# Kernel optimization log

Measured on AMD Instinct MI355X. Metric: run time of the kernel, lower is better.

## Reference

```python
import jax, jax.numpy as jnp
import numpy as np

N_USER = 25000
N_ITEM = 25000
N = N_USER + N_ITEM
E = 1_250_000
D = 64
L = 3
B = 4096


def setup_inputs() -> dict:
    key = jax.random.key(0)
    ks = jax.random.split(key, 11)
    emb = jax.random.normal(ks[0], (N, D), dtype=jnp.float32) * 0.1
    w1_w = jax.random.normal(ks[1], (L, D, D), dtype=jnp.float32) / np.sqrt(D)
    w1_b = jax.random.normal(ks[2], (L, D), dtype=jnp.float32) * 0.01
    w2_w = jax.random.normal(ks[3], (L, D, D), dtype=jnp.float32) / np.sqrt(D)
    w2_b = jax.random.normal(ks[4], (L, D), dtype=jnp.float32) * 0.01
    # normalized-laplacian-like nonneg values
    vals = jax.random.uniform(ks[5], (E,), dtype=jnp.float32) * 0.1
    rows = jax.random.randint(ks[6], (E,), 0, N, dtype=jnp.int32)
    cols = jax.random.randint(ks[7], (E,), 0, N, dtype=jnp.int32)
    user = jax.random.randint(ks[8], (B,), 0, N_USER, dtype=jnp.int32)
    pos = jax.random.randint(ks[9], (B,), 0, N, dtype=jnp.int32)
    neg = jax.random.randint(ks[10], (B,), 0, N, dtype=jnp.int32)
    return {"emb": emb, "w1_w": w1_w, "w1_b": w1_b, "w2_w": w2_w,
            "w2_b": w2_b, "vals": vals, "rows": rows, "cols": cols,
            "user": user, "pos": pos, "neg": neg}


def _spmm(vals, rows, cols, x):
    # sparse [N,N] @ dense [N,D] via gather + segment_sum
    msg = vals[:, None] * x[cols]          # [E, D]
    return jax.ops.segment_sum(msg, rows, num_segments=N)  # [N, D]


def reference(emb, w1_w, w1_b, w2_w, w2_b, vals, rows, cols, user, pos, neg):
    user_embs = [emb[user]]
    pos_embs = [emb[pos]]
    neg_embs = [emb[neg]]
    for l in range(L):
        agg = _spmm(vals, rows, cols, emb)                # sp.mm(laplacian, emb)
        # (laplacian + identity) @ emb == agg + emb
        sx = (agg + emb) @ w1_w[l].T + w1_b[l]
        ox = agg * (emb @ w2_w[l].T + w2_b[l])
        emb = jax.nn.leaky_relu(sx + ox, negative_slope=0.01)
        user_embs.append(emb[user])
        pos_embs.append(emb[pos])
        neg_embs.append(emb[neg])
    user_e = jnp.concatenate(user_embs, axis=-1)          # [B, (L+1)*D]
    pos_e = jnp.concatenate(pos_embs, axis=-1)
    neg_e = jnp.concatenate(neg_embs, axis=-1)
    pos_logits = jnp.einsum('id,id->i', user_e, pos_e)
    neg_logits = jnp.einsum('id,id->i', user_e, neg_e)
    # -log(sigmoid(diff)).sum(), computed stably
    return -jnp.sum(jax.nn.log_sigmoid(pos_logits - neg_logits))
```

## Files before the change

kernel.cpp:

```cpp
#include <hip/hip_runtime.h>
#include <hip/hip_fp16.h>
#include <math.h>

#define N_NODES 50000
#define EDGES   1250000
#define DIM     64
#define NLAYER  3
#define BATCH   4096

#define NBUCK 196
#define RPB   256
#define NABLK 512
#define BCAP  7424

typedef unsigned int uint32;
typedef _Float16 f16x8 __attribute__((ext_vector_type(8)));
typedef float f32x4 __attribute__((ext_vector_type(4)));

static __device__ __forceinline__ ushort f2h(float f) {
    return __half_as_ushort(__float2half(f));
}
static __device__ __forceinline__ float h2f(ushort u) {
    return __half2float(__ushort_as_half(u));
}


#define HP_F2H   512
#define HP_DOTS  3637
#define HP_TOTAL 4661

__global__ __launch_bounds__(256) void histprep_kernel(const int* __restrict__ rows,
                                                       int* __restrict__ bhist,
                                                       const float* __restrict__ emb,
                                                       ushort* __restrict__ xh,
                                                       const int* __restrict__ user,
                                                       const int* __restrict__ pos,
                                                       const int* __restrict__ neg,
                                                       float* __restrict__ dots,
                                                       float* __restrict__ out) {
    __shared__ int h[NBUCK];
    int blk = blockIdx.x;
    int tid = threadIdx.x;
    if (blk < HP_F2H) {
        if (blk == 0 && tid == 0) out[0] = 0.f;
        for (int i = tid; i < NBUCK; i += 256) h[i] = 0;
        __syncthreads();
        int per = (EDGES + NABLK - 1) / NABLK;
        int e0 = blk * per;
        int e1 = min(e0 + per, EDGES);
        for (int e = e0 + tid; e < e1; e += 256)
            atomicAdd(&h[rows[e] >> 8], 1);
        __syncthreads();
        for (int i = tid; i < NBUCK; i += 256)
            bhist[(size_t)i * NABLK + blk] = h[i];
    } else if (blk < HP_DOTS) {
        int i = (blk - HP_F2H) * 256 + tid;
        float4 v = ((const float4*)emb)[i];
        ushort4 hh;
        hh.x = f2h(v.x); hh.y = f2h(v.y); hh.z = f2h(v.z); hh.w = f2h(v.w);
        ((ushort4*)xh)[i] = hh;
    } else {
        int lane = tid & 63;
        int i = (blk - HP_DOTS) * 4 + (tid >> 6);
        int ui = user[i], pi = pos[i], ni = neg[i];
        float u = emb[(size_t)ui * DIM + lane];
        float p = emb[(size_t)pi * DIM + lane];
        float n = emb[(size_t)ni * DIM + lane];
        float v = u * (p - n);
#pragma unroll
        for (int off = 32; off; off >>= 1) v += __shfl_xor(v, off);
        if (lane == 0) dots[i] = v;
    }
}


__global__ __launch_bounds__(512) void boffs_kernel(const int* __restrict__ bhist,
                                                    int* __restrict__ boffs) {
    __shared__ int sbase[256];
    __shared__ int wred[8];
    int b = blockIdx.x;
    int tid = threadIdx.x;
    int lane = tid & 63, wid = tid >> 6;

    int tot = 0;
    if (tid < NBUCK) {
        const int* p = bhist + (size_t)tid * NABLK;
        for (int k = 0; k < NABLK; ++k) tot += p[k];
    }
    int sB = tot;
    if (tid < 256) {
#pragma unroll
        for (int off = 1; off < 64; off <<= 1) {
            int tt = __shfl_up(sB, off);
            if (lane >= off) sB += tt;
        }
        if (lane == 63) wred[wid] = sB;
    }
    __syncthreads();
    if (tid == 0) {
        int a = 0;
#pragma unroll
        for (int i = 0; i < 4; ++i) { int tt = wred[i]; wred[i] = a; a += tt; }
    }
    __syncthreads();
    if (tid < 256) sbase[tid] = wred[wid] + sB - tot;
    __syncthreads();
    int base = sbase[b];
    __syncthreads();

    int v = bhist[(size_t)b * NABLK + tid];
    int s = v;
#pragma unroll
    for (int off = 1; off < 64; off <<= 1) {
        int tt = __shfl_up(s, off);
        if (lane >= off) s += tt;
    }
    if (lane == 63) wred[wid] = s;
    __syncthreads();
    if (tid == 0) {
        int a = 0;
#pragma unroll
        for (int i = 0; i < 8; ++i) { int tt = wred[i]; wred[i] = a; a += tt; }
    }
    __syncthreads();
    boffs[(size_t)b * NABLK + tid] = base + wred[wid] + s - v;
}


__global__ __launch_bounds__(256) void bucket_scatter_kernel(const int* __restrict__ rows,
                                                             const int* __restrict__ cols,
                                                             const float* __restrict__ vals,
                                                             const int* __restrict__ boffs,
                                                             int2* __restrict__ staging) {
    __shared__ int cur[NBUCK];
    for (int t = threadIdx.x; t < NBUCK; t += 256)
        cur[t] = boffs[(size_t)t * NABLK + blockIdx.x];
    __syncthreads();
    int per = (EDGES + NABLK - 1) / NABLK;
    int e0 = blockIdx.x * per;
    int e1 = min(e0 + per, EDGES);
    for (int e = e0 + threadIdx.x; e < e1; e += 256) {
        int r = rows[e];
        int p = atomicAdd(&cur[r >> 8], 1);
        staging[p] = make_int2(((r & 255) << 16) | cols[e], __float_as_int(vals[e]));
    }
}


__global__ __launch_bounds__(512) void csr_build_kernel(const int* __restrict__ boffs,
                                                        const int2* __restrict__ staging,
                                                        int* __restrict__ row_ptr,
                                                        uint32* __restrict__ csr) {
    __shared__ int2 sedge[BCAP];
    __shared__ int rcur[RPB];
    __shared__ int wred[4];
    int b = blockIdx.x;
    int base = boffs[(size_t)b * NABLK];
    int end = (b == NBUCK - 1) ? EDGES : boffs[(size_t)(b + 1) * NABLK];
    int cnt = end - base;
    bool inlds = (cnt <= BCAP);
    int tid = threadIdx.x;
    int lane = tid & 63, wid = tid >> 6;
    if (tid < RPB) rcur[tid] = 0;
    __syncthreads();
    if (inlds) {
        for (int p = tid; p < cnt; p += 512) {
            int2 e = staging[base + p];
            sedge[p] = e;
            atomicAdd(&rcur[e.x >> 16], 1);
        }
    } else {
        for (int p = base + tid; p < end; p += 512)
            atomicAdd(&rcur[staging[p].x >> 16], 1);
    }
    __syncthreads();
    int v = 0, s = 0;
    if (tid < RPB) {
        v = rcur[tid];
        s = v;
#pragma unroll
        for (int off = 1; off < 64; off <<= 1) {
            int t = __shfl_up(s, off);
            if (lane >= off) s += t;
        }
        if (lane == 63) wred[wid] = s;
    }
    __syncthreads();
    if (tid == 0) {
        int a = 0;
#pragma unroll
        for (int i = 0; i < 4; ++i) { int t = wred[i]; wred[i] = a; a += t; }
    }
    __syncthreads();
    if (tid < RPB) {
        int excl = wred[wid] + s - v;
        rcur[tid] = base + excl;
        int row = b * RPB + tid;
        if (row < N_NODES) row_ptr[row] = base + excl;
    }
    if (b == NBUCK - 1 && tid == 0) row_ptr[N_NODES] = EDGES;
    __syncthreads();
    if (inlds) {
        for (int p = tid; p < cnt; p += 512) {
            int2 e = sedge[p];
            int pos = atomicAdd(&rcur[e.x >> 16], 1);
            csr[pos] = ((uint32)(e.x & 0xFFFF) << 16) | (uint32)f2h(__int_as_float(e.y));
        }
    } else {
        for (int p = base + tid; p < end; p += 512) {
            int2 e = staging[p];
            int pos = atomicAdd(&rcur[e.x >> 16], 1);
            csr[pos] = ((uint32)(e.x & 0xFFFF) << 16) | (uint32)f2h(__int_as_float(e.y));
        }
    }
}


__global__ __launch_bounds__(256) void spmm_kernel(const int* __restrict__ row_ptr,
                                                   const uint32* __restrict__ csr,
                                                   const ushort* __restrict__ xh,
                                                   ushort* __restrict__ aggh,
                                                   const int* __restrict__ user,
                                                   const int* __restrict__ pos,
                                                   const int* __restrict__ neg,
                                                   float* __restrict__ dots,
                                                   int nsb) {
    int lane = threadIdx.x & 63;
    if ((int)blockIdx.x >= nsb) {
        int i = (blockIdx.x - nsb) * 4 + (threadIdx.x >> 6);
        int ui = user[i], pi = pos[i], ni = neg[i];
        float u = h2f(xh[(size_t)ui * DIM + lane]);
        float p = h2f(xh[(size_t)pi * DIM + lane]);
        float n = h2f(xh[(size_t)ni * DIM + lane]);
        float v = u * (p - n);
#pragma unroll
        for (int off = 32; off; off >>= 1) v += __shfl_xor(v, off);
        if (lane == 0) dots[i] = v;
        return;
    }
    int g = lane >> 3;
    int sl = lane & 7;
    int row = blockIdx.x * 4 + (threadIdx.x >> 6);
    int p0 = row_ptr[row], p1 = row_ptr[row + 1];
    float a0 = 0, a1 = 0, a2 = 0, a3 = 0, a4 = 0, a5 = 0, a6 = 0, a7 = 0;
    int p = p0;
#define SPMM_ACC(E, X)                                                     \
    {                                                                      \
        float vv = h2f((ushort)((E) & 0xFFFF));                            \
        a0 += vv * h2f((ushort)((X).x & 0xFFFF));                          \
        a1 += vv * h2f((ushort)((X).x >> 16));                             \
        a2 += vv * h2f((ushort)((X).y & 0xFFFF));                          \
        a3 += vv * h2f((ushort)((X).y >> 16));                             \
        a4 += vv * h2f((ushort)((X).z & 0xFFFF));                          \
        a5 += vv * h2f((ushort)((X).z >> 16));                             \
        a6 += vv * h2f((ushort)((X).w & 0xFFFF));                          \
        a7 += vv * h2f((ushort)((X).w >> 16));                             \
    }
    for (; p + 32 <= p1; p += 32) {
        uint32 e0 = csr[p + g];
        uint32 e1 = csr[p + 8 + g];
        uint32 e2 = csr[p + 16 + g];
        uint32 e3 = csr[p + 24 + g];
        uint4 x0 = *(const uint4*)(xh + (size_t)(e0 >> 16) * DIM + sl * 8);
        uint4 x1 = *(const uint4*)(xh + (size_t)(e1 >> 16) * DIM + sl * 8);
        uint4 x2 = *(const uint4*)(xh + (size_t)(e2 >> 16) * DIM + sl * 8);
        uint4 x3 = *(const uint4*)(xh + (size_t)(e3 >> 16) * DIM + sl * 8);
        SPMM_ACC(e0, x0);
        SPMM_ACC(e1, x1);
        SPMM_ACC(e2, x2);
        SPMM_ACC(e3, x3);
    }
    for (; p + 8 <= p1; p += 8) {
        uint32 ea = csr[p + g];
        uint4 xa = *(const uint4*)(xh + (size_t)(ea >> 16) * DIM + sl * 8);
        SPMM_ACC(ea, xa);
    }
    if (p + g < p1) {
        uint32 ea = csr[p + g];
        uint4 xa = *(const uint4*)(xh + (size_t)(ea >> 16) * DIM + sl * 8);
        SPMM_ACC(ea, xa);
    }
#undef SPMM_ACC
#pragma unroll
    for (int m = 8; m <= 32; m <<= 1) {
        a0 += __shfl_xor(a0, m); a1 += __shfl_xor(a1, m);
        a2 += __shfl_xor(a2, m); a3 += __shfl_xor(a3, m);
        a4 += __shfl_xor(a4, m); a5 += __shfl_xor(a5, m);
        a6 += __shfl_xor(a6, m); a7 += __shfl_xor(a7, m);
    }
    if (lane < 8) {
        ushort t[8];
        t[0] = f2h(a0); t[1] = f2h(a1); t[2] = f2h(a2); t[3] = f2h(a3);
        t[4] = f2h(a4); t[5] = f2h(a5); t[6] = f2h(a6); t[7] = f2h(a7);
        *(uint4*)(aggh + (size_t)row * DIM + lane * 8) = *(uint4*)t;
    }
}


__global__ __launch_bounds__(256) void dense_kernel(const ushort* __restrict__ xh_in,
                                                    const ushort* __restrict__ aggh,
                                                    const float* __restrict__ w1,
                                                    const float* __restrict__ w2,
                                                    const float* __restrict__ b1,
                                                    const float* __restrict__ b2,
                                                    ushort* __restrict__ yh) {
    __shared__ ushort xs[64 * 64];
    __shared__ ushort xc[64 * 64];
    __shared__ ushort w1s[64 * 64];
    __shared__ ushort w2s[64 * 64];

    int tid = threadIdx.x;
    int n0 = blockIdx.x * 64;

    {
        int rr = tid >> 2;
        int jq = (tid & 3) << 4;
        int sw = rr & 7;
        int b0 = jq >> 3;
        int o0 = rr * 64 + (((b0 + 0) ^ sw) << 3);
        int o1 = rr * 64 + (((b0 + 1) ^ sw) << 3);

        {
            const float* w1r = w1 + rr * 64 + jq;
            const float* w2r = w2 + rr * 64 + jq;
            ushort t1[16], t2[16];
#pragma unroll
            for (int k = 0; k < 4; ++k) {
                float4 a = ((const float4*)w1r)[k];
                float4 b = ((const float4*)w2r)[k];
                t1[k * 4 + 0] = f2h(a.x); t1[k * 4 + 1] = f2h(a.y);
                t1[k * 4 + 2] = f2h(a.z); t1[k * 4 + 3] = f2h(a.w);
                t2[k * 4 + 0] = f2h(b.x); t2[k * 4 + 1] = f2h(b.y);
                t2[k * 4 + 2] = f2h(b.z); t2[k * 4 + 3] = f2h(b.w);
            }
            *(uint4*)&w1s[o0] = *(uint4*)&t1[0];
            *(uint4*)&w1s[o1] = *(uint4*)&t1[8];
            *(uint4*)&w2s[o0] = *(uint4*)&t2[0];
            *(uint4*)&w2s[o1] = *(uint4*)&t2[8];
        }
        {
            int node = n0 + rr;
            int ncl = (node < N_NODES) ? node : (N_NODES - 1);
            const ushort* ar = aggh + (size_t)ncl * DIM + jq;
            const ushort* xr = xh_in + (size_t)ncl * DIM + jq;
            ushort txs[16], txc[16];
#pragma unroll
            for (int k = 0; k < 2; ++k) {
                uint4 xv = ((const uint4*)xr)[k];
                uint4 av = ((const uint4*)ar)[k];
                uint32 xw[4] = {xv.x, xv.y, xv.z, xv.w};
                uint32 aw[4] = {av.x, av.y, av.z, av.w};
#pragma unroll
                for (int q = 0; q < 4; ++q) {
                    ushort xlo = (ushort)(xw[q] & 0xFFFF);
                    ushort xhi = (ushort)(xw[q] >> 16);
                    ushort alo = (ushort)(aw[q] & 0xFFFF);
                    ushort ahi = (ushort)(aw[q] >> 16);
                    int e = k * 8 + q * 2;
                    txc[e] = xlo; txc[e + 1] = xhi;
                    txs[e] = f2h(h2f(xlo) + h2f(alo));
                    txs[e + 1] = f2h(h2f(xhi) + h2f(ahi));
                }
            }
            *(uint4*)&xs[o0] = *(uint4*)&txs[0];
            *(uint4*)&xs[o1] = *(uint4*)&txs[8];
            *(uint4*)&xc[o0] = *(uint4*)&txc[0];
            *(uint4*)&xc[o1] = *(uint4*)&txc[8];
        }
    }
    __syncthreads();

    int lane = tid & 63, w = tid >> 6;
    int nb = w << 4;
    int lm = lane & 15;
    int le = lane >> 4;

    f16x8 axs[2], axc[2];
#pragma unroll
    for (int k = 0; k < 2; ++k) {
        int n = nb + lm;
        int blk = k * 4 + le;
        int off = n * 64 + ((blk ^ (n & 7)) << 3);
        axs[k] = *(const f16x8*)&xs[off];
        axc[k] = *(const f16x8*)&xc[off];
    }

#pragma unroll
    for (int dt = 0; dt < 4; ++dt) {
        int d = dt * 16 + lm;
        f16x8 bf1[2], bf2[2];
#pragma unroll
        for (int k = 0; k < 2; ++k) {
            int blk = k * 4 + le;
            int off = d * 64 + ((blk ^ (d & 7)) << 3);
            bf1[k] = *(const f16x8*)&w1s[off];
            bf2[k] = *(const f16x8*)&w2s[off];
        }
        f32x4 acc1 = {0.f, 0.f, 0.f, 0.f};
        f32x4 acc2 = {0.f, 0.f, 0.f, 0.f};
        acc1 = __builtin_amdgcn_mfma_f32_16x16x32_f16(axs[0], bf1[0], acc1, 0, 0, 0);
        acc1 = __builtin_amdgcn_mfma_f32_16x16x32_f16(axs[1], bf1[1], acc1, 0, 0, 0);
        acc2 = __builtin_amdgcn_mfma_f32_16x16x32_f16(axc[0], bf2[0], acc2, 0, 0, 0);
        acc2 = __builtin_amdgcn_mfma_f32_16x16x32_f16(axc[1], bf2[1], acc2, 0, 0, 0);

        float b1v = b1[d], b2v = b2[d];
        int bb = d >> 3;
#pragma unroll
        for (int i = 0; i < 4; ++i) {
            int nl = nb + (le << 2) + i;
            int node = n0 + nl;
            int off = nl * 64 + ((bb ^ (nl & 7)) << 3) + (d & 7);
            float ag = h2f(xs[off]) - h2f(xc[off]);
            float t = acc1[i] + b1v + ag * (acc2[i] + b2v);
            t = (t > 0.f) ? t : 0.01f * t;
            if (node < N_NODES) yh[(size_t)node * DIM + d] = f2h(t);
        }
    }
}


__global__ __launch_bounds__(256) void dots_loss_kernel(const ushort* __restrict__ xh,
                                                        const int* __restrict__ user,
                                                        const int* __restrict__ pos,
                                                        const int* __restrict__ neg,
                                                        const float* __restrict__ dots,
                                                        float* __restrict__ out) {
    __shared__ float part[4];
    int tid = threadIdx.x;
    int lane = tid & 63;
    int i = blockIdx.x * 4 + (tid >> 6);
    int ui = user[i], pi = pos[i], ni = neg[i];
    float u = h2f(xh[(size_t)ui * DIM + lane]);
    float p = h2f(xh[(size_t)pi * DIM + lane]);
    float n = h2f(xh[(size_t)ni * DIM + lane]);
    float v = u * (p - n);
#pragma unroll
    for (int off = 32; off; off >>= 1) v += __shfl_xor(v, off);
    if (lane == 0) {
        float d = dots[i] + dots[BATCH + i] + dots[2 * BATCH + i] + v;
        part[tid >> 6] = fmaxf(-d, 0.f) + log1pf(expf(-fabsf(d)));
    }
    __syncthreads();
    if (tid == 0) atomicAdd(out, part[0] + part[1] + part[2] + part[3]);
}


extern "C" void kernel_launch(void* const* d_in, const int* in_sizes, int n_in,
                              void* d_out, int out_size, void* d_ws, size_t ws_size,
                              hipStream_t stream) {
    const float* emb  = (const float*)d_in[0];
    const float* w1_w = (const float*)d_in[1];
    const float* w1_b = (const float*)d_in[2];
    const float* w2_w = (const float*)d_in[3];
    const float* w2_b = (const float*)d_in[4];
    const float* vals = (const float*)d_in[5];
    const int* rows = (const int*)d_in[6];
    const int* cols = (const int*)d_in[7];
    const int* user = (const int*)d_in[8];
    const int* pos  = (const int*)d_in[9];
    const int* neg  = (const int*)d_in[10];
    float* out = (float*)d_out;

    char* w = (char*)d_ws;
    char* region = w;          w += (size_t)N_NODES * DIM * 4;
    ushort* aggh = (ushort*)region;
    int2* staging = (int2*)region;
    int* row_ptr = (int*)w;   w += (((size_t)(N_NODES + 1) * 4) + 255) / 256 * 256;
    uint32* csr  = (uint32*)w; w += (size_t)EDGES * 4;
    int* bhist   = (int*)w;   w += (size_t)NBUCK * NABLK * 4;
    int* boffs   = (int*)w;   w += (size_t)NBUCK * NABLK * 4;
    float* dots  = (float*)w; w += (size_t)3 * BATCH * 4;
    ushort* xhA  = (ushort*)w; w += (size_t)N_NODES * DIM * 2;
    ushort* xhB  = (ushort*)w; w += (size_t)N_NODES * DIM * 2;

    histprep_kernel<<<HP_TOTAL, 256, 0, stream>>>(rows, bhist, emb, xhA,
                                                  user, pos, neg, dots, out);
    boffs_kernel<<<NBUCK, 512, 0, stream>>>(bhist, boffs);
    bucket_scatter_kernel<<<NABLK, 256, 0, stream>>>(rows, cols, vals, boffs, staging);
    csr_build_kernel<<<NBUCK, 512, 0, stream>>>(boffs, staging, row_ptr, csr);

    const int NSB = N_NODES / 4;
    const int NTB = BATCH / 4;
    const int NDB = (N_NODES + 63) / 64;

    spmm_kernel<<<NSB, 256, 0, stream>>>(row_ptr, csr, xhA, aggh, user, pos, neg, dots, NSB);
    dense_kernel<<<NDB, 256, 0, stream>>>(xhA, aggh, w1_w + 0 * 4096, w2_w + 0 * 4096,
                                          w1_b + 0 * DIM, w2_b + 0 * DIM, xhB);
    spmm_kernel<<<NSB + NTB, 256, 0, stream>>>(row_ptr, csr, xhB, aggh, user, pos, neg,
                                               dots + BATCH, NSB);
    dense_kernel<<<NDB, 256, 0, stream>>>(xhB, aggh, w1_w + 1 * 4096, w2_w + 1 * 4096,
                                          w1_b + 1 * DIM, w2_b + 1 * DIM, xhA);
    spmm_kernel<<<NSB + NTB, 256, 0, stream>>>(row_ptr, csr, xhA, aggh, user, pos, neg,
                                               dots + 2 * BATCH, NSB);
    dense_kernel<<<NDB, 256, 0, stream>>>(xhA, aggh, w1_w + 2 * 4096, w2_w + 2 * 4096,
                                          w1_b + 2 * DIM, w2_b + 2 * DIM, xhB);

    dots_loss_kernel<<<NTB, 256, 0, stream>>>(xhB, user, pos, neg, dots, out);
}
```

Measured before the change: 177.6 us.

## Compute final layer only for the batch's user/pos/neg nodes

The last layer's embeddings are only consumed at the 3*B gathered indices, so the final spmm and dense passes now run over 12288 slots instead of all 50000 nodes. Slot-indexed aggregation and output buffers are added, and the loss kernel reads them contiguously. This removes roughly three quarters of the last layer's sparse gather and dense work. Duplicate indices get recomputed per slot, and two new kernel variants are added.

```diff
diff --git a/kernel.cpp b/kernel.cpp
--- a/kernel.cpp
+++ b/kernel.cpp
@@ -7,6 +7,7 @@
 #define DIM     64
 #define NLAYER  3
 #define BATCH   4096
+#define NSLOTS  (3 * BATCH)
 
 #define NBUCK 196
 #define RPB   256
@@ -22,6 +23,15 @@
 }
 static __device__ __forceinline__ float h2f(ushort u) {
     return __half2float(__ushort_as_half(u));
+}
+
+static __device__ __forceinline__ int slot_node(int slot,
+                                                const int* __restrict__ user,
+                                                const int* __restrict__ pos,
+                                                const int* __restrict__ neg) {
+    if (slot < BATCH) return user[slot];
+    if (slot < 2 * BATCH) return pos[slot - BATCH];
+    return neg[slot - 2 * BATCH];
 }
 
 
@@ -216,46 +226,23 @@
 }
 
 
-__global__ __launch_bounds__(256) void spmm_kernel(const int* __restrict__ row_ptr,
-                                                   const uint32* __restrict__ csr,
-                                                   const ushort* __restrict__ xh,
-                                                   ushort* __restrict__ aggh,
-                                                   const int* __restrict__ user,
-                                                   const int* __restrict__ pos,
-                                                   const int* __restrict__ neg,
-                                                   float* __restrict__ dots,
-                                                   int nsb) {
-    int lane = threadIdx.x & 63;
-    if ((int)blockIdx.x >= nsb) {
-        int i = (blockIdx.x - nsb) * 4 + (threadIdx.x >> 6);
-        int ui = user[i], pi = pos[i], ni = neg[i];
-        float u = h2f(xh[(size_t)ui * DIM + lane]);
-        float p = h2f(xh[(size_t)pi * DIM + lane]);
-        float n = h2f(xh[(size_t)ni * DIM + lane]);
-        float v = u * (p - n);
-#pragma unroll
-        for (int off = 32; off; off >>= 1) v += __shfl_xor(v, off);
-        if (lane == 0) dots[i] = v;
-        return;
-    }
-    int g = lane >> 3;
-    int sl = lane & 7;
-    int row = blockIdx.x * 4 + (threadIdx.x >> 6);
-    int p0 = row_ptr[row], p1 = row_ptr[row + 1];
-    float a0 = 0, a1 = 0, a2 = 0, a3 = 0, a4 = 0, a5 = 0, a6 = 0, a7 = 0;
-    int p = p0;
+static __device__ __forceinline__ void spmm_row(const uint32* __restrict__ csr,
+                                                const ushort* __restrict__ xh,
+                                                int p0, int p1, int g, int sl,
+                                                float* a) {
 #define SPMM_ACC(E, X)                                                     \
     {                                                                      \
         float vv = h2f((ushort)((E) & 0xFFFF));                            \
-        a0 += vv * h2f((ushort)((X).x & 0xFFFF));                          \
-        a1 += vv * h2f((ushort)((X).x >> 16));                             \
-        a2 += vv * h2f((ushort)((X).y & 0xFFFF));                          \
-        a3 += vv * h2f((ushort)((X).y >> 16));                             \
-        a4 += vv * h2f((ushort)((X).z & 0xFFFF));                          \
-        a5 += vv * h2f((ushort)((X).z >> 16));                             \
-        a6 += vv * h2f((ushort)((X).w & 0xFFFF));                          \
-        a7 += vv * h2f((ushort)((X).w >> 16));                             \
-    }
+        a[0] += vv * h2f((ushort)((X).x & 0xFFFF));                        \
+        a[1] += vv * h2f((ushort)((X).x >> 16));                           \
+        a[2] += vv * h2f((ushort)((X).y & 0xFFFF));                        \
+        a[3] += vv * h2f((ushort)((X).y >> 16));                           \
+        a[4] += vv * h2f((ushort)((X).z & 0xFFFF));                        \
+        a[5] += vv * h2f((ushort)((X).z >> 16));                           \
+        a[6] += vv * h2f((ushort)((X).w & 0xFFFF));                        \
+        a[7] += vv * h2f((ushort)((X).w >> 16));                           \
+    }
+    int p = p0;
     for (; p + 32 <= p1; p += 32) {
         uint32 e0 = csr[p + g];
         uint32 e1 = csr[p + 8 + g];
@@ -283,27 +270,97 @@
 #undef SPMM_ACC
 #pragma unroll
     for (int m = 8; m <= 32; m <<= 1) {
-        a0 += __shfl_xor(a0, m); a1 += __shfl_xor(a1, m);
-        a2 += __shfl_xor(a2, m); a3 += __shfl_xor(a3, m);
-        a4 += __shfl_xor(a4, m); a5 += __shfl_xor(a5, m);
-        a6 += __shfl_xor(a6, m); a7 += __shfl_xor(a7, m);
-    }
+        a[0] += __shfl_xor(a[0], m); a[1] += __shfl_xor(a[1], m);
+        a[2] += __shfl_xor(a[2], m); a[3] += __shfl_xor(a[3], m);
+        a[4] += __shfl_xor(a[4], m); a[5] += __shfl_xor(a[5], m);
+        a[6] += __shfl_xor(a[6], m); a[7] += __shfl_xor(a[7], m);
+    }
+}
+
+static __device__ __forceinline__ void spmm_store(ushort* dst, const float* a, int lane) {
     if (lane < 8) {
         ushort t[8];
-        t[0] = f2h(a0); t[1] = f2h(a1); t[2] = f2h(a2); t[3] = f2h(a3);
-        t[4] = f2h(a4); t[5] = f2h(a5); t[6] = f2h(a6); t[7] = f2h(a7);
-        *(uint4*)(aggh + (size_t)row * DIM + lane * 8) = *(uint4*)t;
-    }
-}
-
-
-__global__ __launch_bounds__(256) void dense_kernel(const ushort* __restrict__ xh_in,
-                                                    const ushort* __restrict__ aggh,
-                                                    const float* __restrict__ w1,
-                                                    const float* __restrict__ w2,
-                                                    const float* __restrict__ b1,
-                                                    const float* __restrict__ b2,
-                                                    ushort* __restrict__ yh) {
+        t[0] = f2h(a[0]); t[1] = f2h(a[1]); t[2] = f2h(a[2]); t[3] = f2h(a[3]);
+        t[4] = f2h(a[4]); t[5] = f2h(a[5]); t[6] = f2h(a[6]); t[7] = f2h(a[7]);
+        *(uint4*)(dst + lane * 8) = *(uint4*)t;
+    }
+}
+
+static __device__ __forceinline__ void dots_tail(const ushort* __restrict__ xh,
+                                                 const int* __restrict__ user,
+                                                 const int* __restrict__ pos,
+                                                 const int* __restrict__ neg,
+                                                 float* __restrict__ dots,
+                                                 int i, int lane) {
+    int ui = user[i], pi = pos[i], ni = neg[i];
+    float u = h2f(xh[(size_t)ui * DIM + lane]);
+    float p = h2f(xh[(size_t)pi * DIM + lane]);
+    float n = h2f(xh[(size_t)ni * DIM + lane]);
+    float v = u * (p - n);
+#pragma unroll
+    for (int off = 32; off; off >>= 1) v += __shfl_xor(v, off);
+    if (lane == 0) dots[i] = v;
+}
+
+
+__global__ __launch_bounds__(256) void spmm_kernel(const int* __restrict__ row_ptr,
+                                                   const uint32* __restrict__ csr,
+                                                   const ushort* __restrict__ xh,
+                                                   ushort* __restrict__ aggh,
+                                                   const int* __restrict__ user,
+                                                   const int* __restrict__ pos,
+                                                   const int* __restrict__ neg,
+                                                   float* __restrict__ dots,
+                                                   int nsb) {
+    int lane = threadIdx.x & 63;
+    if ((int)blockIdx.x >= nsb) {
+        int i = (blockIdx.x - nsb) * 4 + (threadIdx.x >> 6);
+        dots_tail(xh, user, pos, neg, dots, i, lane);
+        return;
+    }
+    int row = blockIdx.x * 4 + (threadIdx.x >> 6);
+    int p0 = row_ptr[row], p1 = row_ptr[row + 1];
+    float a[8] = {};
+    spmm_row(csr, xh, p0, p1, lane >> 3, lane & 7, a);
+    spmm_store(aggh + (size_t)row * DIM, a, lane);
+}
+
+
+__global__ __launch_bounds__(256) void spmm_slots_kernel(const int* __restrict__ row_ptr,
+                                                         const uint32* __restrict__ csr,
+                                                         const ushort* __restrict__ xh,
+                                                         ushort* __restrict__ aggh_slot,
+                                                         const int* __restrict__ user,
+                                                         const int* __restrict__ pos,
+                                                         const int* __restrict__ neg,
+                                                         float* __restrict__ dots,
+                                                         int nsb) {
+    int lane = threadIdx.x & 63;
+    if ((int)blockIdx.x >= nsb) {
+        int i = (blockIdx.x - nsb) * 4 + (threadIdx.x >> 6);
+        dots_tail(xh, user, pos, neg, dots, i, lane);
+        return;
+    }
+    int slot = blockIdx.x * 4 + (threadIdx.x >> 6);
+    int node = slot_node(slot, user, pos, neg);
+    int p0 = row_ptr[node], p1 = row_ptr[node + 1];
+    float a[8] = {};
+    spmm_row(csr, xh, p0, p1, lane >> 3, lane & 7, a);
+    spmm_store(aggh_slot + (size_t)slot * DIM, a, lane);
+}
+
+
+template <int IS_SLOT>
+static __device__ __forceinline__ void dense_body(const ushort* __restrict__ xh_in,
+                                                  const ushort* __restrict__ aggh,
+                                                  const float* __restrict__ w1,
+                                                  const float* __restrict__ w2,
+                                                  const float* __restrict__ b1,
+                                                  const float* __restrict__ b2,
+                                                  ushort* __restrict__ yh,
+                                                  const int* __restrict__ user,
+                                                  const int* __restrict__ pos,
+                                                  const int* __restrict__ neg) {
     __shared__ ushort xs[64 * 64];
     __shared__ ushort xc[64 * 64];
     __shared__ ushort w1s[64 * 64];
@@ -339,10 +396,17 @@
             *(uint4*)&w2s[o1] = *(uint4*)&t2[8];
         }
         {
-            int node = n0 + rr;
-            int ncl = (node < N_NODES) ? node : (N_NODES - 1);
-            const ushort* ar = aggh + (size_t)ncl * DIM + jq;
-            const ushort* xr = xh_in + (size_t)ncl * DIM + jq;
+            int rowid = n0 + rr;
+            int xnode, arow;
+            if (IS_SLOT) {
+                xnode = slot_node(rowid, user, pos, neg);
+                arow = rowid;
+            } else {
+                xnode = (rowid < N_NODES) ? rowid : (N_NODES - 1);
+                arow = xnode;
+            }
+            const ushort* ar = aggh + (size_t)arow * DIM + jq;
+            const ushort* xr = xh_in + (size_t)xnode * DIM + jq;
             ushort txs[16], txc[16];
 #pragma unroll
             for (int k = 0; k < 2; ++k) {
@@ -408,31 +472,51 @@
 #pragma unroll
         for (int i = 0; i < 4; ++i) {
             int nl = nb + (le << 2) + i;
-            int node = n0 + nl;
+            int rowid = n0 + nl;
             int off = nl * 64 + ((bb ^ (nl & 7)) << 3) + (d & 7);
             float ag = h2f(xs[off]) - h2f(xc[off]);
             float t = acc1[i] + b1v + ag * (acc2[i] + b2v);
             t = (t > 0.f) ? t : 0.01f * t;
-            if (node < N_NODES) yh[(size_t)node * DIM + d] = f2h(t);
-        }
-    }
-}
-
-
-__global__ __launch_bounds__(256) void dots_loss_kernel(const ushort* __restrict__ xh,
-                                                        const int* __restrict__ user,
-                                                        const int* __restrict__ pos,
-                                                        const int* __restrict__ neg,
+            bool wr = IS_SLOT ? true : (rowid < N_NODES);
+            if (wr) yh[(size_t)rowid * DIM + d] = f2h(t);
+        }
+    }
+}
+
+__global__ __launch_bounds__(256) void dense_kernel(const ushort* __restrict__ xh_in,
+                                                    const ushort* __restrict__ aggh,
+                                                    const float* __restrict__ w1,
+                                                    const float* __restrict__ w2,
+                                                    const float* __restrict__ b1,
+                                                    const float* __restrict__ b2,
+                                                    ushort* __restrict__ yh) {
+    dense_body<0>(xh_in, aggh, w1, w2, b1, b2, yh, nullptr, nullptr, nullptr);
+}
+
+__global__ __launch_bounds__(256) void dense_slots_kernel(const ushort* __restrict__ xh_in,
+                                                          const ushort* __restrict__ aggh_slot,
+                                                          const float* __restrict__ w1,
+                                                          const float* __restrict__ w2,
+                                                          const float* __restrict__ b1,
+                                                          const float* __restrict__ b2,
+                                                          ushort* __restrict__ yh_slot,
+                                                          const int* __restrict__ user,
+                                                          const int* __restrict__ pos,
+                                                          const int* __restrict__ neg) {
+    dense_body<1>(xh_in, aggh_slot, w1, w2, b1, b2, yh_slot, user, pos, neg);
+}
+
+
+__global__ __launch_bounds__(256) void dots_loss_kernel(const ushort* __restrict__ yh_slot,
                                                         const float* __restrict__ dots,
                                                         float* __restrict__ out) {
     __shared__ float part[4];
     int tid = threadIdx.x;
     int lane = tid & 63;
     int i = blockIdx.x * 4 + (tid >> 6);
-    int ui = user[i], pi = pos[i], ni = neg[i];
-    float u = h2f(xh[(size_t)ui * DIM + lane]);
-    float p = h2f(xh[(size_t)pi * DIM + lane]);
-    float n = h2f(xh[(size_t)ni * DIM + lane]);
+    float u = h2f(yh_slot[(size_t)i * DIM + lane]);
+    float p = h2f(yh_slot[(size_t)(BATCH + i) * DIM + lane]);
+    float n = h2f(yh_slot[(size_t)(2 * BATCH + i) * DIM + lane]);
     float v = u * (p - n);
 #pragma unroll
     for (int off = 32; off; off >>= 1) v += __shfl_xor(v, off);
@@ -472,6 +556,8 @@
     float* dots  = (float*)w; w += (size_t)3 * BATCH * 4;
     ushort* xhA  = (ushort*)w; w += (size_t)N_NODES * DIM * 2;
     ushort* xhB  = (ushort*)w; w += (size_t)N_NODES * DIM * 2;
+    ushort* aggh_slot = (ushort*)w; w += (size_t)NSLOTS * DIM * 2;
+    ushort* yh_slot   = (ushort*)w; w += (size_t)NSLOTS * DIM * 2;
 
     histprep_kernel<<<HP_TOTAL, 256, 0, stream>>>(rows, bhist, emb, xhA,
                                                   user, pos, neg, dots, out);
@@ -482,6 +568,8 @@
     const int NSB = N_NODES / 4;
     const int NTB = BATCH / 4;
     const int NDB = (N_NODES + 63) / 64;
+    const int NSLB = NSLOTS / 4;
+    const int NSDB = NSLOTS / 64;
 
     spmm_kernel<<<NSB, 256, 0, stream>>>(row_ptr, csr, xhA, aggh, user, pos, neg, dots, NSB);
     dense_kernel<<<NDB, 256, 0, stream>>>(xhA, aggh, w1_w + 0 * 4096, w2_w + 0 * 4096,
@@ -490,10 +578,12 @@
                                                dots + BATCH, NSB);
     dense_kernel<<<NDB, 256, 0, stream>>>(xhB, aggh, w1_w + 1 * 4096, w2_w + 1 * 4096,
                                           w1_b + 1 * DIM, w2_b + 1 * DIM, xhA);
-    spmm_kernel<<<NSB + NTB, 256, 0, stream>>>(row_ptr, csr, xhA, aggh, user, pos, neg,
-                                               dots + 2 * BATCH, NSB);
-    dense_kernel<<<NDB, 256, 0, stream>>>(xhA, aggh, w1_w + 2 * 4096, w2_w + 2 * 4096,
-                                          w1_b + 2 * DIM, w2_b + 2 * DIM, xhB);
-
-    dots_loss_kernel<<<NTB, 256, 0, stream>>>(xhB, user, pos, neg, dots, out);
-}
+    spmm_slots_kernel<<<NSLB + NTB, 256, 0, stream>>>(row_ptr, csr, xhA, aggh_slot,
+                                                      user, pos, neg, dots + 2 * BATCH, NSLB);
+    dense_slots_kernel<<<NSDB, 256, 0, stream>>>(xhA, aggh_slot,
+                                                 w1_w + 2 * 4096, w2_w + 2 * 4096,
+                                                 w1_b + 2 * DIM, w2_b + 2 * DIM,
+                                                 yh_slot, user, pos, neg);
+
+    dots_loss_kernel<<<NTB, 256, 0, stream>>>(yh_slot, dots, out);
+}
```

After: 156.3 us. 12.0% less time.
